# Kernel optimization log

Hardware: AMD Instinct MI355X
Metric: run time of the kernel (lower is better)

Reference implementation:

```python
import jax, jax.numpy as jnp
import numpy as np

N = 100000
E = 1600000
IN_DIM = 128
HID = 128
C = 10
N_INJ = 20000
T_HET = 0.5          # self.hetero_level (set by set_adaptation_from_data)
HP_MAX = 1.0         # highpass_scale_max
INJ_LAM = 0.8        # self.inject_lambda


def setup_inputs() -> dict:
    key = jax.random.key(0)
    ks = jax.random.split(key, 16)
    glorot = lambda k, i, o: jax.random.normal(k, (i, o), jnp.float32) * (2.0 / (i + o)) ** 0.5
    return {
        "x": jax.random.normal(ks[0], (N, IN_DIM), jnp.float32),
        "edge_index": jax.random.randint(ks[1], (2, E), 0, N, jnp.int64),
        "inject_indices": jax.random.randint(ks[2], (N_INJ,), 0, N, jnp.int64),
        "initial_preds": jax.random.uniform(ks[3], (N, C), jnp.float32),
        "W1": glorot(ks[4], IN_DIM, HID), "b1": jnp.zeros((HID,), jnp.float32),
        "W2": glorot(ks[5], HID, HID),   "b2": jnp.zeros((HID,), jnp.float32),
        "Wl1": glorot(ks[6], IN_DIM, HID),
        "Wl2": glorot(ks[7], HID, HID),
        "Wm1": glorot(ks[8], HID, HID), "bm1": jnp.zeros((HID,), jnp.float32),
        "Wm2": glorot(ks[9], HID, C),   "bm2": jnp.zeros((C,), jnp.float32),
    }


def _gcn_norm(edge_index):
    # add self loops, symmetric D^{-1/2} (A+I) D^{-1/2} normalization (PyG GCNConv default)
    loops = jnp.arange(N, dtype=edge_index.dtype)
    src = jnp.concatenate([edge_index[0], loops])
    dst = jnp.concatenate([edge_index[1], loops])
    deg = jax.ops.segment_sum(jnp.ones_like(dst, jnp.float32), dst, num_segments=N)
    dinv = jnp.where(deg > 0, jax.lax.rsqrt(jnp.maximum(deg, 1.0)), 0.0)
    norm = dinv[src] * dinv[dst]  # [E+N]
    return src, dst, norm


def _gcn_conv(x, W, b, src, dst, norm):
    h = x @ W                                   # [N, H]
    msg = h[src] * norm[:, None]                # gather + scale, [E+N, H]
    return jax.ops.segment_sum(msg, dst, num_segments=N) + b


def reference(x, edge_index, inject_indices, initial_preds,
              W1, b1, W2, b2, Wl1, Wl2, Wm1, bm1, Wm2, bm2):
    src, dst, norm = _gcn_norm(edge_index)
    mix = T_HET * HP_MAX

    low1 = _gcn_conv(x, W1, b1, src, dst, norm)
    high1 = x @ Wl1 - low1
    h = jax.nn.relu(low1 + mix * high1)        # dropout: eval mode (identity)

    low2 = _gcn_conv(h, W2, b2, src, dst, norm)
    high2 = h @ Wl2 - low2
    h2 = low2 + mix * high2

    logits = jax.nn.relu(h2 @ Wm1 + bm1) @ Wm2 + bm2   # [N, C]
    # indexed injection: logits[idx] = logits[idx] + lam * preds[idx]
    logits = logits.at[inject_indices].set(
        logits[inject_indices] + INJ_LAM * initial_preds[inject_indices])
    return jax.nn.log_softmax(logits, axis=1)
```

## Files before the change

kernel.cpp:

```cpp
#include <hip/hip_runtime.h>
#include <hip/hip_bf16.h>
#include <math.h>

typedef __attribute__((ext_vector_type(8))) short short8;
typedef __attribute__((ext_vector_type(4))) float f32x4;
typedef __attribute__((ext_vector_type(2))) float f32x2;

#define INJ_LAM 0.8f
#define BSH 9
#define BWD 512

__device__ inline float bf2f(unsigned short s){
  union{unsigned u; float f;} v; v.u=((unsigned)s)<<16; return v.f;
}
__device__ inline unsigned short f2bf(float f){
  __hip_bfloat16 h=__float2bfloat16(f);
  return *reinterpret_cast<unsigned short*>(&h);
}
__device__ inline unsigned pack2(float lo, float hi){
  return ((unsigned)f2bf(hi)<<16)|(unsigned)f2bf(lo);
}

__global__ void k_prep(const float* __restrict__ W1,const float* __restrict__ Wl1,
                       const float* __restrict__ W2,const float* __restrict__ Wl2,
                       const float* __restrict__ Wm1,const float* __restrict__ Wm2,
                       const float* __restrict__ b1,const float* __restrict__ b2,
                       unsigned short* __restrict__ Wt1, unsigned short* __restrict__ Wt2,
                       unsigned short* __restrict__ Wm1t, unsigned short* __restrict__ Wm2tp,
                       float* __restrict__ bh1, float* __restrict__ bh2,
                       unsigned* __restrict__ flags32, int nf4,
                       unsigned* __restrict__ bhist8, unsigned* __restrict__ zcur8){
  int i=blockIdx.x*blockDim.x+threadIdx.x;
  if(i<256*128){
    int c=i>>7, k=i&127;
    float v1=(c<128)?W1[k*128+c]:Wl1[k*128+(c-128)];
    float v2=(c<128)?W2[k*128+c]:Wl2[k*128+(c-128)];
    Wt1[i]=f2bf(v1); Wt2[i]=f2bf(v2);
    if(c<128) Wm1t[i]=f2bf(Wm1[k*128+c]);
    if(c<16)  Wm2tp[i]=f2bf((c<10)?Wm2[k*10+c]:0.f);
    if(i<128){ bh1[i]=0.5f*b1[i]; bh2[i]=0.5f*b2[i]; }
  }
  if(i<nf4) flags32[i]=0u;
  if(i<2048){ bhist8[i]=0u; zcur8[i]=0u; }
}

__global__ void k_bhist(const int* __restrict__ dst, unsigned* __restrict__ bhist8, int E){
  __shared__ unsigned lh[256];
  int t=threadIdx.x;
  lh[t]=0u; __syncthreads();
  int base=blockIdx.x*2048;
  #pragma unroll
  for(int k=0;k<8;k++){
    int e=base+k*256+t;
    if(e<E) atomicAdd(&lh[dst[e]>>BSH],1u);
  }
  __syncthreads();
  if(lh[t]) atomicAdd(&bhist8[t*8],lh[t]);
}

__launch_bounds__(256)
__global__ void k_bscatter(const int* __restrict__ src, const int* __restrict__ dst,
                           const unsigned* __restrict__ bhist8, unsigned* __restrict__ zcur8,
                           int* __restrict__ psrc, int* __restrict__ pdst, int E, int NBK){
  __shared__ unsigned lh[256];
  __shared__ unsigned gb[256];
  __shared__ unsigned ss[256];
  int t=threadIdx.x;
  lh[t]=0u;
  unsigned v=(t<NBK)?bhist8[t*8]:0u;
  ss[t]=v; __syncthreads();
  for(int off=1;off<256;off<<=1){
    unsigned u=(t>=off)?ss[t-off]:0u; __syncthreads();
    ss[t]+=u; __syncthreads();
  }
  unsigned bb=ss[t]-v;
  int base=blockIdx.x*2048;
  unsigned lr[8]; int bk[8], sv[8], dv_[8];
  #pragma unroll
  for(int k=0;k<8;k++){
    int e=base+k*256+t;
    if(e<E){
      int d=dst[e]; int b=d>>BSH;
      bk[k]=b; dv_[k]=d; sv[k]=src[e];
      lr[k]=atomicAdd(&lh[b],1u);
    } else bk[k]=-1;
  }
  __syncthreads();
  if(lh[t]) gb[t]=bb+atomicAdd(&zcur8[t*8],lh[t]);
  __syncthreads();
  #pragma unroll
  for(int k=0;k<8;k++){
    if(bk[k]>=0){
      unsigned p=gb[bk[k]]+lr[k];
      psrc[p]=sv[k]; pdst[p]=dv_[k];
    }
  }
}

__launch_bounds__(256)
__global__ void k_bucket(const int* __restrict__ psrc, const int* __restrict__ pdst,
                         const unsigned* __restrict__ bhist8, unsigned* __restrict__ rank,
                         unsigned* __restrict__ meta, float* __restrict__ dinv,
                         int* __restrict__ csr,
                         const int* __restrict__ inj, unsigned char* __restrict__ flag,
                         int N, int NI, int NBK){
  __shared__ unsigned lc[BWD];
  __shared__ unsigned lo[BWD];
  __shared__ unsigned ss[256];
  int b=blockIdx.x, t=threadIdx.x;
  for(int i=b*256+t;i<NI;i+=gridDim.x*256) flag[inj[i]]=1;
  unsigned v=(t<NBK)?bhist8[t*8]:0u;
  ss[t]=v; lc[t]=0u; lc[t+256]=0u;
  __syncthreads();
  for(int off=1;off<256;off<<=1){
    unsigned u=(t>=off)?ss[t-off]:0u; __syncthreads();
    ss[t]+=u; __syncthreads();
  }
  unsigned e1=ss[b];
  unsigned e0=e1-bhist8[b*8];
  __syncthreads();
  int lo_node=b<<BSH;
  for(unsigned p=e0+t;p<e1;p+=256){
    int dl=pdst[p]-lo_node;
    rank[p]=atomicAdd(&lc[dl],1u);
  }
  __syncthreads();
  unsigned c0=lc[2*t], c1=lc[2*t+1], ps=c0+c1;
  ss[t]=ps; __syncthreads();
  for(int off=1;off<256;off<<=1){
    unsigned u=(t>=off)?ss[t-off]:0u; __syncthreads();
    ss[t]+=u; __syncthreads();
  }
  unsigned excl=ss[t]-ps;
  lo[2*t]=excl; lo[2*t+1]=excl+c0;
  __syncthreads();
  #pragma unroll
  for(int k=0;k<2;k++){
    int nl=t+k*256; int node=lo_node+nl;
    if(node<N){
      unsigned c=lc[nl];
      meta[node]=(e0+lo[nl])|(c<<21);
      dinv[node]=rsqrtf((float)(c+1u));
    }
  }
  for(unsigned p=e0+t;p<e1;p+=256){
    int dl=pdst[p]-lo_node;
    csr[e0+lo[dl]+rank[p]]=psrc[p];
  }
}

template<bool FP32IN>
__device__ inline void load_afrag(const void* __restrict__ Xv, size_t arow, int l4, short8* a){
  if(FP32IN){
    const float* X=(const float*)Xv + arow*128 + l4*8;
    #pragma unroll
    for(int ks=0;ks<4;ks++){
      float4 f0=*reinterpret_cast<const float4*>(X+ks*32);
      float4 f1=*reinterpret_cast<const float4*>(X+ks*32+4);
      short8 t;
      t[0]=(short)f2bf(f0.x); t[1]=(short)f2bf(f0.y); t[2]=(short)f2bf(f0.z); t[3]=(short)f2bf(f0.w);
      t[4]=(short)f2bf(f1.x); t[5]=(short)f2bf(f1.y); t[6]=(short)f2bf(f1.z); t[7]=(short)f2bf(f1.w);
      a[ks]=t;
    }
  }else{
    const unsigned short* X=(const unsigned short*)Xv + arow*128 + l4*8;
    #pragma unroll
    for(int ks=0;ks<4;ks++)
      a[ks]=*reinterpret_cast<const short8*>(X+ks*32);
  }
}

template<bool FP32IN>
__launch_bounds__(256, 4)
__global__ void k_gemm(const void* __restrict__ Xv, const unsigned short* __restrict__ Wt,
                       const float* __restrict__ dinv,
                       unsigned short* __restrict__ G, unsigned short* __restrict__ XL, int N){
  int wave=threadIdx.x>>6, lane=threadIdx.x&63;
  int l15=lane&15, l4=lane>>4;
  int blk0=blockIdx.x*128;
  if(blk0>=N) return;
  short8 wf[4][4];
  #pragma unroll
  for(int i=0;i<4;i++){
    int col=(wave*4+i)*16+l15;
    #pragma unroll
    for(int ks=0;ks<4;ks++)
      wf[i][ks]=*reinterpret_cast<const short8*>(Wt+(size_t)col*128+ks*32+l4*8);
  }
  int r0=blk0+l15; if(r0>N-1) r0=N-1;
  short8 aC[4], aN[4];
  load_afrag<FP32IN>(Xv,(size_t)r0,l4,aC);
  #pragma unroll 1
  for(int nt=0;nt<8;nt++){
    int node0=blk0+nt*16;
    if(node0>=N) break;
    if(nt<7){
      int rn=node0+16+l15; if(rn>N-1) rn=N-1;
      load_afrag<FP32IN>(Xv,(size_t)rn,l4,aN);
    }
    f32x4 acc[4];
    #pragma unroll
    for(int i=0;i<4;i++) acc[i]=(f32x4){0.f,0.f,0.f,0.f};
    #pragma unroll
    for(int i=0;i<4;i++){
      #pragma unroll
      for(int ks=0;ks<4;ks++)
        acc[i]=__builtin_amdgcn_mfma_f32_16x16x32_bf16(wf[i][ks],aC[ks],acc[i],0,0,0);
    }
    int node=node0+l15;
    if(node<N){
      if(wave<2){
        float dv=dinv[node];
        #pragma unroll
        for(int i=0;i<4;i++){
          f32x4 v=acc[i];
          uint2 p; p.x=pack2(v[0]*dv,v[1]*dv); p.y=pack2(v[2]*dv,v[3]*dv);
          *reinterpret_cast<uint2*>(G+(size_t)node*128+(wave*4+i)*16+l4*4)=p;
        }
      }else{
        #pragma unroll
        for(int i=0;i<4;i++){
          f32x4 v=acc[i];
          uint2 p; p.x=pack2(v[0]*0.5f,v[1]*0.5f); p.y=pack2(v[2]*0.5f,v[3]*0.5f);
          *reinterpret_cast<uint2*>(XL+(size_t)node*128+((wave-2)*4+i)*16+l4*4)=p;
        }
      }
    }
    #pragma unroll
    for(int ks=0;ks<4;ks++) aC[ks]=aN[ks];
  }
}

#define ADDQ(v) do{ \
  unsigned ux=(unsigned)(v).x, uy=(unsigned)(v).y, uz=(unsigned)(v).z, uw=(unsigned)(v).w; \
  accv[0]+=(f32x2){__uint_as_float(ux<<16),__uint_as_float(ux&0xffff0000u)}; \
  accv[1]+=(f32x2){__uint_as_float(uy<<16),__uint_as_float(uy&0xffff0000u)}; \
  accv[2]+=(f32x2){__uint_as_float(uz<<16),__uint_as_float(uz&0xffff0000u)}; \
  accv[3]+=(f32x2){__uint_as_float(uw<<16),__uint_as_float(uw&0xffff0000u)}; \
}while(0)

template<bool RELU>
__device__ __forceinline__ void conv_node(int node, int N,
    const unsigned short* __restrict__ G, const unsigned short* __restrict__ XL,
    const float* __restrict__ bh, const float* __restrict__ dinv,
    const int* __restrict__ csr, const unsigned* __restrict__ meta,
    unsigned short* __restrict__ ldsrow, int lane){
  if(node>=N) return;
  int g=lane>>4, li=lane&15;
  const int4* Gv=(const int4*)G;
  const int4 Z={0,0,0,0};
  f32x2 accv[4];
  #pragma unroll
  for(int i=0;i<4;i++) accv[i]=(f32x2){0.f,0.f};
  if(g==0){
    int4 v=Gv[(size_t)node*16+li];
    ADDQ(v);
  }
  unsigned mt=meta[node];
  unsigned start=mt&0x1FFFFFu, deg=mt>>21;
  unsigned j=(unsigned)g;
  int4 v0=Z,v1=Z,v2=Z,v3=Z;
  if(j<deg)    v0=Gv[(size_t)csr[start+j]*16+li];
  if(j+4<deg)  v1=Gv[(size_t)csr[start+j+4]*16+li];
  if(j+8<deg)  v2=Gv[(size_t)csr[start+j+8]*16+li];
  if(j+12<deg) v3=Gv[(size_t)csr[start+j+12]*16+li];
  j+=16;
  while(j<deg){
    int4 n0=Z,n1=Z,n2=Z,n3=Z;
    n0=Gv[(size_t)csr[start+j]*16+li];
    if(j+4<deg)  n1=Gv[(size_t)csr[start+j+4]*16+li];
    if(j+8<deg)  n2=Gv[(size_t)csr[start+j+8]*16+li];
    if(j+12<deg) n3=Gv[(size_t)csr[start+j+12]*16+li];
    ADDQ(v0); ADDQ(v1); ADDQ(v2); ADDQ(v3);
    v0=n0; v1=n1; v2=n2; v3=n3; j+=16;
  }
  ADDQ(v0); ADDQ(v1); ADDQ(v2); ADDQ(v3);
  float acc[8];
  #pragma unroll
  for(int i=0;i<4;i++){ acc[2*i]=accv[i][0]; acc[2*i+1]=accv[i][1]; }
  #pragma unroll
  for(int i=0;i<8;i++){
    acc[i]+=__shfl_xor(acc[i],16,64);
    acc[i]+=__shfl_xor(acc[i],32,64);
  }
  if(g==0){
    float dv2=0.5f*dinv[node];
    float4 b0=*reinterpret_cast<const float4*>(bh+li*8);
    float4 b1=*reinterpret_cast<const float4*>(bh+li*8+4);
    int4 xv=((const int4*)XL)[(size_t)node*16+li];
    float xl[8];
    { unsigned _x=(unsigned)xv.x,_y=(unsigned)xv.y,_z=(unsigned)xv.z,_w=(unsigned)xv.w;
      xl[0]=bf2f((unsigned short)(_x&0xffffu)); xl[1]=bf2f((unsigned short)(_x>>16));
      xl[2]=bf2f((unsigned short)(_y&0xffffu)); xl[3]=bf2f((unsigned short)(_y>>16));
      xl[4]=bf2f((unsigned short)(_z&0xffffu)); xl[5]=bf2f((unsigned short)(_z>>16));
      xl[6]=bf2f((unsigned short)(_w&0xffffu)); xl[7]=bf2f((unsigned short)(_w>>16)); }
    float bb[8]={b0.x,b0.y,b0.z,b0.w,b1.x,b1.y,b1.z,b1.w};
    float r[8];
    #pragma unroll
    for(int i=0;i<8;i++){
      r[i]=dv2*acc[i]+bb[i]+xl[i];
      if(RELU) r[i]=fmaxf(r[i],0.f);
    }
    int4 o;
    o.x=(int)pack2(r[0],r[1]); o.y=(int)pack2(r[2],r[3]);
    o.z=(int)pack2(r[4],r[5]); o.w=(int)pack2(r[6],r[7]);
    *reinterpret_cast<int4*>(ldsrow+li*8)=o;
  }
}

__launch_bounds__(512, 4)
__global__ void k_convg(const unsigned short* __restrict__ G1, const unsigned short* __restrict__ XL1,
                        const float* __restrict__ bh1, const float* __restrict__ dinv,
                        const int* __restrict__ csr, const unsigned* __restrict__ meta,
                        const unsigned short* __restrict__ Wt2,
                        unsigned short* __restrict__ G2, unsigned short* __restrict__ XL2, int N){
  __shared__ __align__(16) unsigned short ht[32][136];
  int wave=threadIdx.x>>6, lane=threadIdx.x&63;
  int l15=lane&15, l4=lane>>4;
  int blk0=blockIdx.x*32;
  #pragma unroll 1
  for(int it=0;it<4;it++){
    int nl=it*8+wave;
    conv_node<true>(blk0+nl, N, G1, XL1, bh1, dinv, csr, meta, &ht[nl][0], lane);
  }
  short8 wf[2][4];
  #pragma unroll
  for(int i=0;i<2;i++){
    int col=(wave+i*8)*16+l15;
    #pragma unroll
    for(int ks=0;ks<4;ks++)
      wf[i][ks]=*reinterpret_cast<const short8*>(Wt2+(size_t)col*128+ks*32+l4*8);
  }
  __syncthreads();
  #pragma unroll
  for(int q=0;q<2;q++){
    short8 a[4];
    #pragma unroll
    for(int ks=0;ks<4;ks++)
      a[ks]=*reinterpret_cast<const short8*>(&ht[q*16+l15][ks*32+l4*8]);
    int node=blk0+q*16+l15;
    float dv=(node<N)?dinv[node]:0.f;
    #pragma unroll
    for(int i=0;i<2;i++){
      f32x4 acc=(f32x4){0.f,0.f,0.f,0.f};
      #pragma unroll
      for(int ks=0;ks<4;ks++)
        acc=__builtin_amdgcn_mfma_f32_16x16x32_bf16(wf[i][ks],a[ks],acc,0,0,0);
      if(node<N){
        int ct=wave+i*8;
        if(ct<8){
          uint2 p; p.x=pack2(acc[0]*dv,acc[1]*dv); p.y=pack2(acc[2]*dv,acc[3]*dv);
          *reinterpret_cast<uint2*>(G2+(size_t)node*128+ct*16+l4*4)=p;
        }else{
          uint2 p; p.x=pack2(acc[0]*0.5f,acc[1]*0.5f); p.y=pack2(acc[2]*0.5f,acc[3]*0.5f);
          *reinterpret_cast<uint2*>(XL2+(size_t)node*128+(ct-8)*16+l4*4)=p;
        }
      }
    }
  }
}

__launch_bounds__(512, 4)
__global__ void k_convm(const unsigned short* __restrict__ G2, const unsigned short* __restrict__ XL2,
                        const float* __restrict__ bh2, const float* __restrict__ dinv,
                        const int* __restrict__ csr, const unsigned* __restrict__ meta,
                        const unsigned short* __restrict__ Wm1t, const unsigned short* __restrict__ Wm2tp,
                        const float* __restrict__ bm1, const float* __restrict__ bm2,
                        const unsigned char* __restrict__ flag, const float* __restrict__ preds,
                        float* __restrict__ out, int N){
  __shared__ __align__(16) unsigned short ht[32][136];
  __shared__ __align__(16) unsigned short zt[32][136];
  int wave=threadIdx.x>>6, lane=threadIdx.x&63;
  int l15=lane&15, l4=lane>>4;
  int blk0=blockIdx.x*32;
  #pragma unroll 1
  for(int it=0;it<4;it++){
    int nl=it*8+wave;
    conv_node<false>(blk0+nl, N, G2, XL2, bh2, dinv, csr, meta, &ht[nl][0], lane);
  }
  short8 wf1[4];
  {
    int col=wave*16+l15;
    #pragma unroll
    for(int ks=0;ks<4;ks++)
      wf1[ks]=*reinterpret_cast<const short8*>(Wm1t+(size_t)col*128+ks*32+l4*8);
  }
  __syncthreads();
  #pragma unroll
  for(int q=0;q<2;q++){
    short8 a[4];
    #pragma unroll
    for(int ks=0;ks<4;ks++)
      a[ks]=*reinterpret_cast<const short8*>(&ht[q*16+l15][ks*32+l4*8]);
    f32x4 acc=(f32x4){0.f,0.f,0.f,0.f};
    #pragma unroll
    for(int ks=0;ks<4;ks++)
      acc=__builtin_amdgcn_mfma_f32_16x16x32_bf16(wf1[ks],a[ks],acc,0,0,0);
    float4 bm=*reinterpret_cast<const float4*>(bm1+wave*16+l4*4);
    uint2 p;
    p.x=pack2(fmaxf(acc[0]+bm.x,0.f),fmaxf(acc[1]+bm.y,0.f));
    p.y=pack2(fmaxf(acc[2]+bm.z,0.f),fmaxf(acc[3]+bm.w,0.f));
    *reinterpret_cast<uint2*>(&zt[q*16+l15][wave*16+l4*4])=p;
  }
  __syncthreads();
  if(wave<2){
    int q=wave;
    short8 a2[4], w2[4];
    #pragma unroll
    for(int ks=0;ks<4;ks++){
      a2[ks]=*reinterpret_cast<const short8*>(&zt[q*16+l15][ks*32+l4*8]);
      w2[ks]=*reinterpret_cast<const short8*>(Wm2tp+(size_t)l15*128+ks*32+l4*8);
    }
    f32x4 acc2=(f32x4){0.f,0.f,0.f,0.f};
    #pragma unroll
    for(int ks=0;ks<4;ks++)
      acc2=__builtin_amdgcn_mfma_f32_16x16x32_bf16(w2[ks],a2[ks],acc2,0,0,0);
    int node=blk0+q*16+l15;
    bool have=node<N;
    int c0=l4*4;
    float v[4];
    #pragma unroll
    for(int k=0;k<4;k++){
      int c=c0+k;
      v[k]=(c<10)?(acc2[k]+bm2[c]):-3.0e38f;
    }
    if(have && c0<10 && flag[node]){
      #pragma unroll
      for(int k=0;k<4;k++){
        int c=c0+k;
        if(c<10) v[k]+=INJ_LAM*preds[(size_t)node*10+c];
      }
    }
    float m=fmaxf(fmaxf(v[0],v[1]),fmaxf(v[2],v[3]));
    m=fmaxf(m,__shfl_xor(m,16,64));
    m=fmaxf(m,__shfl_xor(m,32,64));
    float s=0.f;
    #pragma unroll
    for(int k=0;k<4;k++){ int c=c0+k; if(c<10) s+=expf(v[k]-m); }
    s+=__shfl_xor(s,16,64);
    s+=__shfl_xor(s,32,64);
    float lse=m+logf(s);
    if(have && c0<10){
      float2 o01; o01.x=v[0]-lse; o01.y=v[1]-lse;
      *reinterpret_cast<float2*>(out+(size_t)node*10+c0)=o01;
      if(c0+2<10){
        float2 o23; o23.x=v[2]-lse; o23.y=v[3]-lse;
        *reinterpret_cast<float2*>(out+(size_t)node*10+c0+2)=o23;
      }
    }
  }
}

extern "C" void kernel_launch(void* const* d_in, const int* in_sizes, int n_in,
                              void* d_out, int out_size, void* d_ws, size_t ws_size,
                              hipStream_t stream){
  const float* x    =(const float*)d_in[0];
  const int*   ei   =(const int*)  d_in[1];
  const int*   inj  =(const int*)  d_in[2];
  const float* preds=(const float*)d_in[3];
  const float* W1 =(const float*)d_in[4];  const float* b1 =(const float*)d_in[5];
  const float* W2 =(const float*)d_in[6];  const float* b2 =(const float*)d_in[7];
  const float* Wl1=(const float*)d_in[8];  const float* Wl2=(const float*)d_in[9];
  const float* Wm1=(const float*)d_in[10]; const float* bm1=(const float*)d_in[11];
  const float* Wm2=(const float*)d_in[12]; const float* bm2=(const float*)d_in[13];
  float* out=(float*)d_out;

  const int N  = in_sizes[0]/128;
  const int E  = in_sizes[1]/2;
  const int NI = in_sizes[2];
  const int* srcp = ei;
  const int* dstp = ei+E;
  const int NBK = (N+BWD-1)>>BSH;

  char* w=(char*)d_ws;
  auto carve=[&](size_t sz)->char*{ char* p=w; w+=(sz+255)&~(size_t)255; return p; };
  unsigned short* S1 =(unsigned short*)carve((size_t)N*128*2);
  unsigned short* S2 =(unsigned short*)carve((size_t)N*128*2);
  unsigned short* S3 =(unsigned short*)carve((size_t)N*128*2);
  unsigned short* Wt1=(unsigned short*)carve(256*128*2);
  unsigned short* Wt2=(unsigned short*)carve(256*128*2);
  unsigned short* Wm1t=(unsigned short*)carve(128*128*2);
  unsigned short* Wm2tp=(unsigned short*)carve(16*128*2);
  float*    dinv  =(float*)   carve((size_t)N*4);
  unsigned* meta  =(unsigned*)carve((size_t)N*4);
  int*      csr   =(int*)     carve((size_t)E*4);
  unsigned char* flags=(unsigned char*)carve(((size_t)N+3)&~(size_t)3);
  unsigned* bhist8=(unsigned*)carve(256*8*4);
  unsigned* zcur8 =(unsigned*)carve(256*8*4);
  float* bh1=(float*)carve(128*4);
  float* bh2=(float*)carve(128*4);
  (void)ws_size; (void)n_in; (void)out_size;

  int* psrc=(int*)S3;
  int* pdst=psrc+E;
  unsigned* rank=(unsigned*)S1;

  const int T=256;
  const int EB=(E+2047)/2048;
  const int nf4=(N+3)/4;
  int gp=(32768>nf4?32768:nf4); gp=(gp+T-1)/T;
  hipLaunchKernelGGL(k_prep, dim3(gp), dim3(T), 0, stream,
                     W1,Wl1,W2,Wl2,Wm1,Wm2,b1,b2,
                     Wt1,Wt2,Wm1t,Wm2tp,bh1,bh2,
                     (unsigned*)flags, nf4, bhist8, zcur8);
  hipLaunchKernelGGL(k_bhist, dim3(EB), dim3(T), 0, stream, dstp, bhist8, E);
  hipLaunchKernelGGL(k_bscatter, dim3(EB), dim3(T), 0, stream, srcp, dstp, bhist8, zcur8,
                     psrc, pdst, E, NBK);
  hipLaunchKernelGGL(k_bucket, dim3(NBK), dim3(T), 0, stream, psrc, pdst, bhist8, rank,
                     meta, dinv, csr, inj, flags, N, NI, NBK);
  hipLaunchKernelGGL(k_gemm<true>, dim3((N+127)/128), dim3(T), 0, stream,
                     (const void*)x, Wt1, dinv, S1, S2, N);
  hipLaunchKernelGGL(k_convg, dim3((N+31)/32), dim3(512), 0, stream,
                     S1, S2, bh1, dinv, csr, meta, Wt2, S2, S3, N);
  hipLaunchKernelGGL(k_convm, dim3((N+31)/32), dim3(512), 0, stream,
                     S2, S3, bh2, dinv, csr, meta, Wm1t, Wm2tp, bm1, bm2,
                     flags, preds, out, N);
}
```

Before: 332.1 us.

## Assign one node per 16-lane group in conv gather, shrink blocks to 16 nodes

The neighbor aggregation now gives each node to a 16-lane quarter-wave, so a wave works on four nodes at once. Before, a whole wave served one node and split its edges across four lane groups, then combined the partial sums with cross-lane shuffles. The shuffle reduction goes away, and a 64-lane wave no longer idles on nodes with few neighbors (about 17 including the self loop). Blocks shrink to 256 threads and 16 nodes, and the follow-on MFMA stages reload weight fragments per column tile. The trade-offs: per-lane memory parallelism per node drops, and nodes in the same wave with uneven degrees cause divergence.

```diff
diff --git a/kernel.cpp b/kernel.cpp
--- a/kernel.cpp
+++ b/kernel.cpp
@@ -240,127 +240,104 @@
 }while(0)
 
 template<bool RELU>
-__device__ __forceinline__ void conv_node(int node, int N,
+__device__ __forceinline__ void conv_group(int node, int N,
     const unsigned short* __restrict__ G, const unsigned short* __restrict__ XL,
     const float* __restrict__ bh, const float* __restrict__ dinv,
     const int* __restrict__ csr, const unsigned* __restrict__ meta,
-    unsigned short* __restrict__ ldsrow, int lane){
+    unsigned short* __restrict__ ldsrow, int li){
   if(node>=N) return;
-  int g=lane>>4, li=lane&15;
   const int4* Gv=(const int4*)G;
   const int4 Z={0,0,0,0};
   f32x2 accv[4];
   #pragma unroll
   for(int i=0;i<4;i++) accv[i]=(f32x2){0.f,0.f};
-  if(g==0){
-    int4 v=Gv[(size_t)node*16+li];
-    ADDQ(v);
-  }
+  { int4 v=Gv[(size_t)node*16+li]; ADDQ(v); }
   unsigned mt=meta[node];
   unsigned start=mt&0x1FFFFFu, deg=mt>>21;
-  unsigned j=(unsigned)g;
   int4 v0=Z,v1=Z,v2=Z,v3=Z;
-  if(j<deg)    v0=Gv[(size_t)csr[start+j]*16+li];
-  if(j+4<deg)  v1=Gv[(size_t)csr[start+j+4]*16+li];
-  if(j+8<deg)  v2=Gv[(size_t)csr[start+j+8]*16+li];
-  if(j+12<deg) v3=Gv[(size_t)csr[start+j+12]*16+li];
-  j+=16;
+  if(0u<deg) v0=Gv[(size_t)csr[start  ]*16+li];
+  if(1u<deg) v1=Gv[(size_t)csr[start+1]*16+li];
+  if(2u<deg) v2=Gv[(size_t)csr[start+2]*16+li];
+  if(3u<deg) v3=Gv[(size_t)csr[start+3]*16+li];
+  unsigned j=4;
   while(j<deg){
-    int4 n0=Z,n1=Z,n2=Z,n3=Z;
-    n0=Gv[(size_t)csr[start+j]*16+li];
-    if(j+4<deg)  n1=Gv[(size_t)csr[start+j+4]*16+li];
-    if(j+8<deg)  n2=Gv[(size_t)csr[start+j+8]*16+li];
-    if(j+12<deg) n3=Gv[(size_t)csr[start+j+12]*16+li];
+    int4 n0=Gv[(size_t)csr[start+j]*16+li];
+    int4 n1=(j+1<deg)?Gv[(size_t)csr[start+j+1]*16+li]:Z;
+    int4 n2=(j+2<deg)?Gv[(size_t)csr[start+j+2]*16+li]:Z;
+    int4 n3=(j+3<deg)?Gv[(size_t)csr[start+j+3]*16+li]:Z;
     ADDQ(v0); ADDQ(v1); ADDQ(v2); ADDQ(v3);
-    v0=n0; v1=n1; v2=n2; v3=n3; j+=16;
+    v0=n0; v1=n1; v2=n2; v3=n3; j+=4;
   }
   ADDQ(v0); ADDQ(v1); ADDQ(v2); ADDQ(v3);
   float acc[8];
   #pragma unroll
   for(int i=0;i<4;i++){ acc[2*i]=accv[i][0]; acc[2*i+1]=accv[i][1]; }
+  float dv2=0.5f*dinv[node];
+  float4 b0=*reinterpret_cast<const float4*>(bh+li*8);
+  float4 b1=*reinterpret_cast<const float4*>(bh+li*8+4);
+  int4 xv=((const int4*)XL)[(size_t)node*16+li];
+  float xl[8];
+  { unsigned _x=(unsigned)xv.x,_y=(unsigned)xv.y,_z=(unsigned)xv.z,_w=(unsigned)xv.w;
+    xl[0]=bf2f((unsigned short)(_x&0xffffu)); xl[1]=bf2f((unsigned short)(_x>>16));
+    xl[2]=bf2f((unsigned short)(_y&0xffffu)); xl[3]=bf2f((unsigned short)(_y>>16));
+    xl[4]=bf2f((unsigned short)(_z&0xffffu)); xl[5]=bf2f((unsigned short)(_z>>16));
+    xl[6]=bf2f((unsigned short)(_w&0xffffu)); xl[7]=bf2f((unsigned short)(_w>>16)); }
+  float bb[8]={b0.x,b0.y,b0.z,b0.w,b1.x,b1.y,b1.z,b1.w};
+  float r[8];
   #pragma unroll
   for(int i=0;i<8;i++){
-    acc[i]+=__shfl_xor(acc[i],16,64);
-    acc[i]+=__shfl_xor(acc[i],32,64);
-  }
-  if(g==0){
-    float dv2=0.5f*dinv[node];
-    float4 b0=*reinterpret_cast<const float4*>(bh+li*8);
-    float4 b1=*reinterpret_cast<const float4*>(bh+li*8+4);
-    int4 xv=((const int4*)XL)[(size_t)node*16+li];
-    float xl[8];
-    { unsigned _x=(unsigned)xv.x,_y=(unsigned)xv.y,_z=(unsigned)xv.z,_w=(unsigned)xv.w;
-      xl[0]=bf2f((unsigned short)(_x&0xffffu)); xl[1]=bf2f((unsigned short)(_x>>16));
-      xl[2]=bf2f((unsigned short)(_y&0xffffu)); xl[3]=bf2f((unsigned short)(_y>>16));
-      xl[4]=bf2f((unsigned short)(_z&0xffffu)); xl[5]=bf2f((unsigned short)(_z>>16));
-      xl[6]=bf2f((unsigned short)(_w&0xffffu)); xl[7]=bf2f((unsigned short)(_w>>16)); }
-    float bb[8]={b0.x,b0.y,b0.z,b0.w,b1.x,b1.y,b1.z,b1.w};
-    float r[8];
-    #pragma unroll
-    for(int i=0;i<8;i++){
-      r[i]=dv2*acc[i]+bb[i]+xl[i];
-      if(RELU) r[i]=fmaxf(r[i],0.f);
-    }
-    int4 o;
-    o.x=(int)pack2(r[0],r[1]); o.y=(int)pack2(r[2],r[3]);
-    o.z=(int)pack2(r[4],r[5]); o.w=(int)pack2(r[6],r[7]);
-    *reinterpret_cast<int4*>(ldsrow+li*8)=o;
-  }
-}
-
-__launch_bounds__(512, 4)
+    r[i]=dv2*acc[i]+bb[i]+xl[i];
+    if(RELU) r[i]=fmaxf(r[i],0.f);
+  }
+  int4 o;
+  o.x=(int)pack2(r[0],r[1]); o.y=(int)pack2(r[2],r[3]);
+  o.z=(int)pack2(r[4],r[5]); o.w=(int)pack2(r[6],r[7]);
+  *reinterpret_cast<int4*>(ldsrow+li*8)=o;
+}
+
+__launch_bounds__(256, 6)
 __global__ void k_convg(const unsigned short* __restrict__ G1, const unsigned short* __restrict__ XL1,
                         const float* __restrict__ bh1, const float* __restrict__ dinv,
                         const int* __restrict__ csr, const unsigned* __restrict__ meta,
                         const unsigned short* __restrict__ Wt2,
                         unsigned short* __restrict__ G2, unsigned short* __restrict__ XL2, int N){
-  __shared__ __align__(16) unsigned short ht[32][136];
+  __shared__ __align__(16) unsigned short ht[16][136];
   int wave=threadIdx.x>>6, lane=threadIdx.x&63;
   int l15=lane&15, l4=lane>>4;
-  int blk0=blockIdx.x*32;
-  #pragma unroll 1
-  for(int it=0;it<4;it++){
-    int nl=it*8+wave;
-    conv_node<true>(blk0+nl, N, G1, XL1, bh1, dinv, csr, meta, &ht[nl][0], lane);
-  }
-  short8 wf[2][4];
-  #pragma unroll
-  for(int i=0;i<2;i++){
-    int col=(wave+i*8)*16+l15;
-    #pragma unroll
-    for(int ks=0;ks<4;ks++)
-      wf[i][ks]=*reinterpret_cast<const short8*>(Wt2+(size_t)col*128+ks*32+l4*8);
-  }
-  __syncthreads();
-  #pragma unroll
-  for(int q=0;q<2;q++){
-    short8 a[4];
-    #pragma unroll
-    for(int ks=0;ks<4;ks++)
-      a[ks]=*reinterpret_cast<const short8*>(&ht[q*16+l15][ks*32+l4*8]);
-    int node=blk0+q*16+l15;
-    float dv=(node<N)?dinv[node]:0.f;
-    #pragma unroll
-    for(int i=0;i<2;i++){
-      f32x4 acc=(f32x4){0.f,0.f,0.f,0.f};
-      #pragma unroll
-      for(int ks=0;ks<4;ks++)
-        acc=__builtin_amdgcn_mfma_f32_16x16x32_bf16(wf[i][ks],a[ks],acc,0,0,0);
-      if(node<N){
-        int ct=wave+i*8;
-        if(ct<8){
-          uint2 p; p.x=pack2(acc[0]*dv,acc[1]*dv); p.y=pack2(acc[2]*dv,acc[3]*dv);
-          *reinterpret_cast<uint2*>(G2+(size_t)node*128+ct*16+l4*4)=p;
-        }else{
-          uint2 p; p.x=pack2(acc[0]*0.5f,acc[1]*0.5f); p.y=pack2(acc[2]*0.5f,acc[3]*0.5f);
-          *reinterpret_cast<uint2*>(XL2+(size_t)node*128+(ct-8)*16+l4*4)=p;
-        }
+  int blk0=blockIdx.x*16;
+  int nl=wave*4+l4;
+  conv_group<true>(blk0+nl, N, G1, XL1, bh1, dinv, csr, meta, &ht[nl][0], l15);
+  __syncthreads();
+  short8 a[4];
+  #pragma unroll
+  for(int ks=0;ks<4;ks++)
+    a[ks]=*reinterpret_cast<const short8*>(&ht[l15][ks*32+l4*8]);
+  int node=blk0+l15;
+  float dv=(node<N)?dinv[node]:0.f;
+  #pragma unroll
+  for(int i=0;i<4;i++){
+    int ct=wave*4+i;
+    short8 wfr[4];
+    #pragma unroll
+    for(int ks=0;ks<4;ks++)
+      wfr[ks]=*reinterpret_cast<const short8*>(Wt2+(size_t)(ct*16+l15)*128+ks*32+l4*8);
+    f32x4 acc=(f32x4){0.f,0.f,0.f,0.f};
+    #pragma unroll
+    for(int ks=0;ks<4;ks++)
+      acc=__builtin_amdgcn_mfma_f32_16x16x32_bf16(wfr[ks],a[ks],acc,0,0,0);
+    if(node<N){
+      if(ct<8){
+        uint2 p; p.x=pack2(acc[0]*dv,acc[1]*dv); p.y=pack2(acc[2]*dv,acc[3]*dv);
+        *reinterpret_cast<uint2*>(G2+(size_t)node*128+ct*16+l4*4)=p;
+      }else{
+        uint2 p; p.x=pack2(acc[0]*0.5f,acc[1]*0.5f); p.y=pack2(acc[2]*0.5f,acc[3]*0.5f);
+        *reinterpret_cast<uint2*>(XL2+(size_t)node*128+(ct-8)*16+l4*4)=p;
       }
     }
   }
 }
 
-__launch_bounds__(512, 4)
+__launch_bounds__(256, 6)
 __global__ void k_convm(const unsigned short* __restrict__ G2, const unsigned short* __restrict__ XL2,
                         const float* __restrict__ bh2, const float* __restrict__ dinv,
                         const int* __restrict__ csr, const unsigned* __restrict__ meta,
@@ -368,54 +345,48 @@
                         const float* __restrict__ bm1, const float* __restrict__ bm2,
                         const unsigned char* __restrict__ flag, const float* __restrict__ preds,
                         float* __restrict__ out, int N){
-  __shared__ __align__(16) unsigned short ht[32][136];
-  __shared__ __align__(16) unsigned short zt[32][136];
+  __shared__ __align__(16) unsigned short ht[16][136];
+  __shared__ __align__(16) unsigned short zt[16][136];
   int wave=threadIdx.x>>6, lane=threadIdx.x&63;
   int l15=lane&15, l4=lane>>4;
-  int blk0=blockIdx.x*32;
-  #pragma unroll 1
-  for(int it=0;it<4;it++){
-    int nl=it*8+wave;
-    conv_node<false>(blk0+nl, N, G2, XL2, bh2, dinv, csr, meta, &ht[nl][0], lane);
-  }
-  short8 wf1[4];
-  {
-    int col=wave*16+l15;
-    #pragma unroll
-    for(int ks=0;ks<4;ks++)
-      wf1[ks]=*reinterpret_cast<const short8*>(Wm1t+(size_t)col*128+ks*32+l4*8);
-  }
-  __syncthreads();
-  #pragma unroll
-  for(int q=0;q<2;q++){
-    short8 a[4];
-    #pragma unroll
-    for(int ks=0;ks<4;ks++)
-      a[ks]=*reinterpret_cast<const short8*>(&ht[q*16+l15][ks*32+l4*8]);
+  int blk0=blockIdx.x*16;
+  int nl=wave*4+l4;
+  conv_group<false>(blk0+nl, N, G2, XL2, bh2, dinv, csr, meta, &ht[nl][0], l15);
+  __syncthreads();
+  short8 a[4];
+  #pragma unroll
+  for(int ks=0;ks<4;ks++)
+    a[ks]=*reinterpret_cast<const short8*>(&ht[l15][ks*32+l4*8]);
+  #pragma unroll
+  for(int i=0;i<2;i++){
+    int ct=wave*2+i;
+    short8 wfr[4];
+    #pragma unroll
+    for(int ks=0;ks<4;ks++)
+      wfr[ks]=*reinterpret_cast<const short8*>(Wm1t+(size_t)(ct*16+l15)*128+ks*32+l4*8);
     f32x4 acc=(f32x4){0.f,0.f,0.f,0.f};
     #pragma unroll
     for(int ks=0;ks<4;ks++)
-      acc=__builtin_amdgcn_mfma_f32_16x16x32_bf16(wf1[ks],a[ks],acc,0,0,0);
-    float4 bm=*reinterpret_cast<const float4*>(bm1+wave*16+l4*4);
+      acc=__builtin_amdgcn_mfma_f32_16x16x32_bf16(wfr[ks],a[ks],acc,0,0,0);
+    float4 bm=*reinterpret_cast<const float4*>(bm1+ct*16+l4*4);
     uint2 p;
     p.x=pack2(fmaxf(acc[0]+bm.x,0.f),fmaxf(acc[1]+bm.y,0.f));
     p.y=pack2(fmaxf(acc[2]+bm.z,0.f),fmaxf(acc[3]+bm.w,0.f));
-    *reinterpret_cast<uint2*>(&zt[q*16+l15][wave*16+l4*4])=p;
-  }
-  __syncthreads();
-  if(wave<2){
-    int q=wave;
+    *reinterpret_cast<uint2*>(&zt[l15][ct*16+l4*4])=p;
+  }
+  __syncthreads();
+  if(wave==0){
     short8 a2[4], w2[4];
     #pragma unroll
     for(int ks=0;ks<4;ks++){
-      a2[ks]=*reinterpret_cast<const short8*>(&zt[q*16+l15][ks*32+l4*8]);
+      a2[ks]=*reinterpret_cast<const short8*>(&zt[l15][ks*32+l4*8]);
       w2[ks]=*reinterpret_cast<const short8*>(Wm2tp+(size_t)l15*128+ks*32+l4*8);
     }
     f32x4 acc2=(f32x4){0.f,0.f,0.f,0.f};
     #pragma unroll
     for(int ks=0;ks<4;ks++)
       acc2=__builtin_amdgcn_mfma_f32_16x16x32_bf16(w2[ks],a2[ks],acc2,0,0,0);
-    int node=blk0+q*16+l15;
+    int node=blk0+l15;
     bool have=node<N;
     int c0=l4*4;
     float v[4];
@@ -510,9 +481,9 @@
                      meta, dinv, csr, inj, flags, N, NI, NBK);
   hipLaunchKernelGGL(k_gemm<true>, dim3((N+127)/128), dim3(T), 0, stream,
                      (const void*)x, Wt1, dinv, S1, S2, N);
-  hipLaunchKernelGGL(k_convg, dim3((N+31)/32), dim3(512), 0, stream,
+  hipLaunchKernelGGL(k_convg, dim3((N+15)/16), dim3(T), 0, stream,
                      S1, S2, bh1, dinv, csr, meta, Wt2, S2, S3, N);
-  hipLaunchKernelGGL(k_convm, dim3((N+31)/32), dim3(512), 0, stream,
+  hipLaunchKernelGGL(k_convm, dim3((N+15)/16), dim3(T), 0, stream,
                      S2, S3, bh2, dinv, csr, meta, Wm1t, Wm2tp, bm1, bm2,
                      flags, preds, out, N);
 }
```

Measured after the change: 327.4 us. Within noise of the previous version (-1.4%).
